# Kernel optimization log

Hardware: AMD Instinct MI355X
Metric: run time of the kernel (lower is better)

Reference implementation:

```python
import jax, jax.numpy as jnp
import numpy as np

N, F, H, C = 50000, 128, 4, 32   # nodes, in_channels, heads, hidden_channels
E, R, DE = 800000, 8, 64         # edges, num_relations, edge_dim


def setup_inputs() -> dict:
    key = jax.random.key(0)
    ks = jax.random.split(key, 10)
    x = jax.random.normal(ks[0], (N, F), dtype=jnp.float32)
    edge_index = jax.random.randint(ks[1], (2, E), 0, N, dtype=jnp.int64)
    edge_type = jax.random.randint(ks[2], (E,), 0, R, dtype=jnp.int64)
    s_in = 1.0 / np.sqrt(F)
    s_e = 1.0 / np.sqrt(DE)
    edge_emb = jax.random.normal(ks[3], (R, DE), dtype=jnp.float32)
    Wq = jax.random.normal(ks[4], (F, H * C), dtype=jnp.float32) * s_in
    Wk = jax.random.normal(ks[5], (F, H * C), dtype=jnp.float32) * s_in
    Wv = jax.random.normal(ks[6], (F, H * C), dtype=jnp.float32) * s_in
    We = jax.random.normal(ks[7], (DE, H * C), dtype=jnp.float32) * s_e
    Wskip = jax.random.normal(ks[8], (F, H * C), dtype=jnp.float32) * s_in
    return {"x": x, "edge_index": edge_index, "edge_type": edge_type,
            "edge_emb": edge_emb, "Wq": Wq, "Wk": Wk, "Wv": Wv,
            "We": We, "Wskip": Wskip}


def reference(x, edge_index, edge_type, edge_emb, Wq, Wk, Wv, We, Wskip):
    # TransformerConv (PyG) with edge embeddings, concat heads, root skip, no bias.
    src, dst = edge_index[0], edge_index[1]
    q = (x @ Wq).reshape(N, H, C)
    k = (x @ Wk).reshape(N, H, C)
    v = (x @ Wv).reshape(N, H, C)
    e = (edge_emb[edge_type] @ We).reshape(E, H, C)      # per-edge relation emb
    kj = k[src] + e                                       # [E,H,C]
    logits = (q[dst] * kj).sum(-1) / jnp.sqrt(jnp.float32(C))  # [E,H]
    # segment softmax over incoming edges of each target node
    m = jax.ops.segment_max(logits, dst, num_segments=N)  # [N,H]
    m = jnp.where(jnp.isfinite(m), m, jnp.float32(0.0))
    ex = jnp.exp(logits - m[dst])
    denom = jax.ops.segment_sum(ex, dst, num_segments=N)  # [N,H]
    alpha = ex / (denom[dst] + 1e-16)                     # [E,H]
    msg = (v[src] + e) * alpha[:, :, None]                # [E,H,C]
    out = jax.ops.segment_sum(msg, dst, num_segments=N).reshape(N, H * C)
    return out + x @ Wskip
```

## Files before the change

### kernel.cpp

```cpp
#include <hip/hip_runtime.h>
#include <hip/hip_bf16.h>

#define NN 50000
#define FF 128
#define NH 4
#define CH 32
#define HC 128
#define NE 800000
#define NR 8
#define DEDIM 64
#define NBLK 196
#define HBLK 3125
#define QBLK 250
#define MTILES 3125

typedef __hip_bfloat16 bf16;
typedef __attribute__((ext_vector_type(8))) short short8;
typedef __attribute__((ext_vector_type(4))) float f32x4;

__device__ __forceinline__ float bflo(unsigned u) { return __uint_as_float(u << 16); }
__device__ __forceinline__ float bfhi(unsigned u) { return __uint_as_float(u & 0xFFFF0000u); }

__device__ __forceinline__ unsigned short f2bf(float f) {
  unsigned u = __float_as_uint(f);
  unsigned r = (u + 0x7FFFu + ((u >> 16) & 1u)) >> 16;
  return (unsigned short)r;
}
__device__ __forceinline__ unsigned pack2bf(float lo, float hi) {
  return (unsigned)f2bf(lo) | ((unsigned)f2bf(hi) << 16);
}

template <int ISBF>
__device__ __forceinline__ float ldf(const void* p, size_t i) {
  if (ISBF) return __bfloat162float(((const bf16*)p)[i]);
  return ((const float*)p)[i];
}

__device__ __forceinline__ int idx_at(const void* p, long long i, int is64) {
  if (is64) { long long v = ((const long long*)p)[i]; return (int)v; }
  return ((const int*)p)[i];
}

#define WT_STRIDE 136

template <int ISBF>
__device__ __forceinline__ void stage_w(const void* __restrict__ W,
                                        unsigned short* __restrict__ wt) {
  for (int i = threadIdx.x; i < FF * HC; i += 256) {
    int k = i >> 7, n = i & 127;
    wt[n * WT_STRIDE + k] = ISBF ? ((const unsigned short*)W)[i]
                                 : f2bf(((const float*)W)[i]);
  }
}

__device__ __forceinline__ void hoist_b(const unsigned short* __restrict__ wt,
                                        int wv, int quad, int lr,
                                        short8 bf[2][4]) {
#pragma unroll
  for (int t = 0; t < 2; ++t) {
    int ncol = wv * 32 + t * 16 + lr;
#pragma unroll
    for (int kb = 0; kb < 4; ++kb)
      bf[t][kb] = *(const short8*)&wt[ncol * WT_STRIDE + kb * 32 + quad * 8];
  }
}

template <int ISBF>
__device__ __forceinline__ void qkvs_body(const void* __restrict__ x,
    const void* __restrict__ W0, const void* __restrict__ W1, int grp, int mc,
    unsigned short* __restrict__ qb, unsigned* __restrict__ kvb,
    void* __restrict__ out, unsigned short* wt) {
  const int lane = threadIdx.x & 63;
  const int wv   = threadIdx.x >> 6;
  const int quad = lane >> 4;
  const int lr   = lane & 15;
  short8 bf0[2][4], bf1[2][4];
  stage_w<ISBF>(W0, wt);
  __syncthreads();
  hoist_b(wt, wv, quad, lr, bf0);
  __syncthreads();
  stage_w<ISBF>(W1, wt);
  __syncthreads();
  hoist_b(wt, wv, quad, lr, bf1);
  const unsigned short* xu = (const unsigned short*)x;
  const float* xf = (const float*)x;
  for (int mt = mc; mt < MTILES; mt += QBLK) {
    int m0 = mt * 16;
    short8 af[4];
#pragma unroll
    for (int kb = 0; kb < 4; ++kb) {
      size_t off = (size_t)(m0 + lr) * FF + kb * 32 + quad * 8;
      if (ISBF) {
        af[kb] = *(const short8*)(xu + off);
      } else {
        float4 fa = *(const float4*)(xf + off);
        float4 fb = *(const float4*)(xf + off + 4);
        short8 a;
        a[0] = (short)f2bf(fa.x); a[1] = (short)f2bf(fa.y);
        a[2] = (short)f2bf(fa.z); a[3] = (short)f2bf(fa.w);
        a[4] = (short)f2bf(fb.x); a[5] = (short)f2bf(fb.y);
        a[6] = (short)f2bf(fb.z); a[7] = (short)f2bf(fb.w);
        af[kb] = a;
      }
    }
    f32x4 a00 = {0.f, 0.f, 0.f, 0.f}, a01 = {0.f, 0.f, 0.f, 0.f};
    f32x4 a10 = {0.f, 0.f, 0.f, 0.f}, a11 = {0.f, 0.f, 0.f, 0.f};
#pragma unroll
    for (int kb = 0; kb < 4; ++kb) {
      a00 = __builtin_amdgcn_mfma_f32_16x16x32_bf16(af[kb], bf0[0][kb], a00, 0, 0, 0);
      a01 = __builtin_amdgcn_mfma_f32_16x16x32_bf16(af[kb], bf0[1][kb], a01, 0, 0, 0);
      a10 = __builtin_amdgcn_mfma_f32_16x16x32_bf16(af[kb], bf1[0][kb], a10, 0, 0, 0);
      a11 = __builtin_amdgcn_mfma_f32_16x16x32_bf16(af[kb], bf1[1][kb], a11, 0, 0, 0);
    }
#pragma unroll
    for (int t = 0; t < 2; ++t) {
      const f32x4 v0 = t ? a01 : a00;
      const f32x4 v1 = t ? a11 : a10;
      int col = wv * 32 + t * 16 + lr;
#pragma unroll
      for (int r = 0; r < 4; ++r) {
        size_t oi = (size_t)(m0 + quad * 4 + r) * HC + col;
        if (grp == 0) {
          qb[oi] = f2bf(v0[r]);
          if (ISBF) ((unsigned short*)out)[oi] = f2bf(v1[r]);
          else      ((float*)out)[oi] = v1[r];
        } else {
          kvb[oi] = pack2bf(v0[r], v1[r]);
        }
      }
    }
  }
}

__global__ __launch_bounds__(256) void k_fusedA(const unsigned* __restrict__ xw,
    const int* __restrict__ eidx32, const void* __restrict__ etype,
    const void* __restrict__ emb, const void* __restrict__ We,
    const void* __restrict__ Wq, const void* __restrict__ Ws,
    int* __restrict__ flag, int* __restrict__ hist, float* __restrict__ ee,
    unsigned* __restrict__ drk, int* __restrict__ setp,
    unsigned short* __restrict__ qb, void* __restrict__ out) {
  __shared__ unsigned short wt[HC * WT_STRIDE];
  if (blockIdx.x < QBLK) {
    unsigned ex = (xw[threadIdx.x & 63] >> 7) & 0xFFu;
    unsigned long long bb = __ballot(ex < 90u || ex > 140u);
    int isbf = (bb == 0ULL);
    if (isbf) qkvs_body<1>(xw, Wq, Ws, 0, blockIdx.x, qb, nullptr, out, wt);
    else      qkvs_body<0>(xw, Wq, Ws, 0, blockIdx.x, qb, nullptr, out, wt);
    return;
  }
  if (blockIdx.x < QBLK + HBLK) {
    unsigned long long b = __ballot(eidx32[2 * (threadIdx.x & 63) + 1] != 0);
    int is64 = (b == 0ULL);
    int e = (blockIdx.x - QBLK) * 256 + threadIdx.x;
    int src = idx_at(eidx32, e, is64);
    int dst = idx_at(eidx32, (long long)NE + e, is64);
    int et  = idx_at(etype, e, is64);
    src = min(max(src, 0), NN - 1);
    dst = min(max(dst, 0), NN - 1);
    et  = min(max(et, 0), NR - 1);
    int rank = atomicAdd(&hist[dst], 1);
    drk[e]  = ((unsigned)dst << 16) | ((unsigned)rank & 0xFFFFu);
    setp[e] = (src << 3) | et;
    return;
  }
  float* es = (float*)wt;
  __shared__ int nzIdx, badBf;
  if (threadIdx.x == 0) { nzIdx = 0; badBf = 0; }
  __syncthreads();
  if (threadIdx.x < 128) {
    if (eidx32[2 * threadIdx.x + 1] != 0) atomicAdd(&nzIdx, 1);
    unsigned e = (xw[threadIdx.x] >> 7) & 0xFFu;
    if (e < 90u || e > 140u) atomicAdd(&badBf, 1);
  }
  __syncthreads();
  const int isbf = (badBf == 0);
  if (threadIdx.x == 0) { flag[0] = (nzIdx == 0); flag[1] = isbf; }
  for (int i = threadIdx.x; i < NR * DEDIM; i += 256)
    es[i] = isbf ? ldf<1>(emb, i) : ldf<0>(emb, i);
  __syncthreads();
  for (int o = threadIdx.x; o < NR * HC; o += 256) {
    int r = o >> 7, j = o & 127;
    float acc = 0.f;
    if (isbf) { for (int d = 0; d < DEDIM; ++d) acc += es[r * DEDIM + d] * ldf<1>(We, d * HC + j); }
    else      { for (int d = 0; d < DEDIM; ++d) acc += es[r * DEDIM + d] * ldf<0>(We, d * HC + j); }
    ee[o] = acc;
  }
}

__global__ __launch_bounds__(256) void k_scan1(const int* __restrict__ hist,
                                               int* __restrict__ bsum) {
  __shared__ int red[4];
  int i = blockIdx.x * 256 + threadIdx.x;
  int v = (i < NN) ? hist[i] : 0;
#pragma unroll
  for (int m = 1; m < 64; m <<= 1) v += __shfl_xor(v, m);
  if ((threadIdx.x & 63) == 0) red[threadIdx.x >> 6] = v;
  __syncthreads();
  if (threadIdx.x == 0) bsum[blockIdx.x] = red[0] + red[1] + red[2] + red[3];
}

__global__ __launch_bounds__(256) void k_scan13(const int* __restrict__ hist,
    const int* __restrict__ bsum, int* __restrict__ rowptr) {
  __shared__ int s[256];
  int t = threadIdx.x;
  int bv = (t < NBLK) ? bsum[t] : 0;
  s[t] = bv;
  __syncthreads();
  for (int off = 1; off < 256; off <<= 1) {
    int u = (t >= off) ? s[t - off] : 0;
    __syncthreads();
    s[t] += u;
    __syncthreads();
  }
  int bexc = (blockIdx.x == 0) ? 0 : s[blockIdx.x - 1];
  __syncthreads();
  int i = blockIdx.x * 256 + t;
  int v = (i < NN) ? hist[i] : 0;
  s[t] = v;
  __syncthreads();
  for (int off = 1; off < 256; off <<= 1) {
    int u = (t >= off) ? s[t - off] : 0;
    __syncthreads();
    s[t] += u;
    __syncthreads();
  }
  int excl = bexc + s[t] - v;
  if (i < NN) rowptr[i] = excl;
  if (i == 0) rowptr[NN] = NE;
}

__global__ __launch_bounds__(256) void k_fusedB(const unsigned* __restrict__ xw,
    const void* __restrict__ Wk, const void* __restrict__ Wv,
    unsigned* __restrict__ kvb,
    const unsigned* __restrict__ drk, const int* __restrict__ setp,
    const int* __restrict__ rowptr, int* __restrict__ srcet) {
  __shared__ unsigned short wt[HC * WT_STRIDE];
  if (blockIdx.x < QBLK) {
    unsigned ex = (xw[threadIdx.x & 63] >> 7) & 0xFFu;
    unsigned long long bb = __ballot(ex < 90u || ex > 140u);
    int isbf = (bb == 0ULL);
    if (isbf) qkvs_body<1>(xw, Wk, Wv, 1, blockIdx.x, nullptr, kvb, nullptr, wt);
    else      qkvs_body<0>(xw, Wk, Wv, 1, blockIdx.x, nullptr, kvb, nullptr, wt);
    return;
  }
  int e = (blockIdx.x - QBLK) * 256 + threadIdx.x;
  unsigned d = drk[e];
  int pos = rowptr[d >> 16] + (int)(d & 0xFFFFu);
  pos = min(max(pos, 0), NE - 1);
  srcet[pos] = setp[e];
}

__global__ __launch_bounds__(256) void k_gather(const int* __restrict__ rowptr,
    const int* __restrict__ srcet, const unsigned short* __restrict__ qb,
    const unsigned* __restrict__ kvb, const float* __restrict__ ee,
    const int* __restrict__ flag, void* __restrict__ out) {
  int n = blockIdx.x * 4 + (threadIdx.x >> 6);
  int l = threadIdx.x & 63;
  int t = l >> 5;
  int w = l & 31;
  int j0 = ((w >> 3) << 5) + ((w & 7) << 2);
  int beg = __builtin_amdgcn_readfirstlane(rowptr[n]);
  int end = __builtin_amdgcn_readfirstlane(rowptr[n + 1]);
  uint2 qw = *(const uint2*)(qb + (size_t)n * HC + j0);
  float q0 = bflo(qw.x), q1 = bfhi(qw.x), q2 = bflo(qw.y), q3 = bfhi(qw.y);
  const float sc = 0.17677669529663687f;
  float dn = 0.f, a0 = 0.f, a1 = 0.f, a2 = 0.f, a3 = 0.f;
  int p = beg;
  for (; p + 8 <= end; p += 8) {
    int se[4]; uint4 kv[4]; float4 ev[4];
#pragma unroll
    for (int u = 0; u < 4; ++u) se[u] = srcet[p + 2 * u + t];
#pragma unroll
    for (int u = 0; u < 4; ++u)
      kv[u] = *(const uint4*)(kvb + (size_t)(se[u] >> 3) * HC + j0);
#pragma unroll
    for (int u = 0; u < 4; ++u)
      ev[u] = *(const float4*)(ee + ((se[u] & 7) << 7) + j0);
#pragma unroll
    for (int u = 0; u < 4; ++u) {
      float pp = q0 * (bflo(kv[u].x) + ev[u].x) + q1 * (bflo(kv[u].y) + ev[u].y)
               + q2 * (bflo(kv[u].z) + ev[u].z) + q3 * (bflo(kv[u].w) + ev[u].w);
      pp += __shfl_xor(pp, 1);
      pp += __shfl_xor(pp, 2);
      pp += __shfl_xor(pp, 4);
      float xx = __expf(pp * sc);
      dn += xx;
      a0 += (bfhi(kv[u].x) + ev[u].x) * xx;
      a1 += (bfhi(kv[u].y) + ev[u].y) * xx;
      a2 += (bfhi(kv[u].z) + ev[u].z) * xx;
      a3 += (bfhi(kv[u].w) + ev[u].w) * xx;
    }
  }
  if (p < end) {
    int se[4]; bool ok[4]; uint4 kv[4]; float4 ev[4];
#pragma unroll
    for (int u = 0; u < 4; ++u) {
      int pe = p + 2 * u + t;
      ok[u] = pe < end;
      se[u] = srcet[ok[u] ? pe : beg];
    }
#pragma unroll
    for (int u = 0; u < 4; ++u)
      kv[u] = *(const uint4*)(kvb + (size_t)(se[u] >> 3) * HC + j0);
#pragma unroll
    for (int u = 0; u < 4; ++u)
      ev[u] = *(const float4*)(ee + ((se[u] & 7) << 7) + j0);
#pragma unroll
    for (int u = 0; u < 4; ++u) {
      float pp = q0 * (bflo(kv[u].x) + ev[u].x) + q1 * (bflo(kv[u].y) + ev[u].y)
               + q2 * (bflo(kv[u].z) + ev[u].z) + q3 * (bflo(kv[u].w) + ev[u].w);
      pp += __shfl_xor(pp, 1);
      pp += __shfl_xor(pp, 2);
      pp += __shfl_xor(pp, 4);
      float xx = ok[u] ? __expf(pp * sc) : 0.f;
      dn += xx;
      a0 += (bfhi(kv[u].x) + ev[u].x) * xx;
      a1 += (bfhi(kv[u].y) + ev[u].y) * xx;
      a2 += (bfhi(kv[u].z) + ev[u].z) * xx;
      a3 += (bfhi(kv[u].w) + ev[u].w) * xx;
    }
  }
  dn += __shfl_xor(dn, 32);
  a0 += __shfl_xor(a0, 32);
  a1 += __shfl_xor(a1, 32);
  a2 += __shfl_xor(a2, 32);
  a3 += __shfl_xor(a3, 32);
  if (t == 0) {
    float inv = 1.f / (dn + 1e-16f);
    size_t oi = (size_t)n * HC + j0;
    if (flag[1]) {
      uint2 sk = *(const uint2*)((const unsigned short*)out + oi);
      uint2 o;
      o.x = pack2bf(a0 * inv + bflo(sk.x), a1 * inv + bfhi(sk.x));
      o.y = pack2bf(a2 * inv + bflo(sk.y), a3 * inv + bfhi(sk.y));
      *(uint2*)((unsigned short*)out + oi) = o;
    } else {
      float4 sk = *(const float4*)((const float*)out + oi);
      float4 o = make_float4(a0 * inv + sk.x, a1 * inv + sk.y,
                             a2 * inv + sk.z, a3 * inv + sk.w);
      *(float4*)((float*)out + oi) = o;
    }
  }
}

extern "C" void kernel_launch(void* const* d_in, const int* in_sizes, int n_in,
                              void* d_out, int out_size, void* d_ws, size_t ws_size,
                              hipStream_t stream) {
  const void* x     = d_in[0];
  const void* eidx  = d_in[1];
  const void* etype = d_in[2];
  const void* emb   = d_in[3];
  const void* Wq    = d_in[4];
  const void* Wk    = d_in[5];
  const void* Wv    = d_in[6];
  const void* We    = d_in[7];
  const void* Ws    = d_in[8];

  float* base   = (float*)d_ws;
  int*   flag   = (int*)base;
  float* ee     = base + 16;
  int*   rowptr = (int*)(base + 1040);
  int*   hist   = (int*)(base + 51044);
  int*   bsum   = (int*)(base + 101044);
  int*   srcet  = (int*)(base + 101568);
  unsigned* drk = (unsigned*)(base + 901568);
  int*   setp   = (int*)(base + 1701568);
  unsigned short* qb  = (unsigned short*)(base + 2501568);
  unsigned*       kvb = (unsigned*)(base + 5701568);

  hipMemsetAsync(hist, 0, NN * sizeof(int), stream);
  k_fusedA<<<QBLK + HBLK + 1, 256, 0, stream>>>((const unsigned*)x,
                                                (const int*)eidx, etype, emb, We,
                                                Wq, Ws, flag, hist, ee,
                                                drk, setp, qb, d_out);
  k_scan1 <<<NBLK, 256, 0, stream>>>(hist, bsum);
  k_scan13<<<NBLK, 256, 0, stream>>>(hist, bsum, rowptr);
  k_fusedB<<<QBLK + HBLK, 256, 0, stream>>>((const unsigned*)x, Wk, Wv, kvb,
                                            drk, setp, rowptr, srcet);
  k_gather<<<NN / 4, 256, 0, stream>>>(rowptr, srcet, qb, kvb, ee, flag, d_out);
}
```

Baseline: 245.0 us.

## Stage GEMM output tiles in LDS for coalesced stores; vectorize weight staging; more projection blocks

The projection GEMM epilogue now writes each 16-row output tile into shared memory and then copies it to global memory with 16-byte coalesced stores, instead of issuing scattered 2- and 4-byte stores per accumulator element. Weight staging into shared memory now uses vectorized copies in row-major layout, and the B-fragment hoist gathers 8 strided scalars per fragment from that layout. The number of projection blocks rises from 250 to 625, which spreads the tiles across more blocks but adds a weight-staging pass to each extra block. The extra barriers per tile and the unpadded, strided LDS reads in the hoist may cause bank conflicts.

```diff
diff --git a/kernel.cpp b/kernel.cpp
--- a/kernel.cpp
+++ b/kernel.cpp
@@ -11,7 +11,7 @@
 #define DEDIM 64
 #define NBLK 196
 #define HBLK 3125
-#define QBLK 250
+#define QBLK 625
 #define MTILES 3125
 
 typedef __hip_bfloat16 bf16;
@@ -41,15 +41,25 @@
   return ((const int*)p)[i];
 }
 
-#define WT_STRIDE 136
-
 template <int ISBF>
 __device__ __forceinline__ void stage_w(const void* __restrict__ W,
                                         unsigned short* __restrict__ wt) {
-  for (int i = threadIdx.x; i < FF * HC; i += 256) {
-    int k = i >> 7, n = i & 127;
-    wt[n * WT_STRIDE + k] = ISBF ? ((const unsigned short*)W)[i]
-                                 : f2bf(((const float*)W)[i]);
+  if (ISBF) {
+    const uint4* src = (const uint4*)W;
+    uint4* dst = (uint4*)wt;
+    for (int i = threadIdx.x; i < FF * HC / 8; i += 256) dst[i] = src[i];
+  } else {
+    const float4* src = (const float4*)W;
+    short8* dst = (short8*)wt;
+    for (int i = threadIdx.x; i < FF * HC / 8; i += 256) {
+      float4 a = src[2 * i], b = src[2 * i + 1];
+      short8 o;
+      o[0] = (short)f2bf(a.x); o[1] = (short)f2bf(a.y);
+      o[2] = (short)f2bf(a.z); o[3] = (short)f2bf(a.w);
+      o[4] = (short)f2bf(b.x); o[5] = (short)f2bf(b.y);
+      o[6] = (short)f2bf(b.z); o[7] = (short)f2bf(b.w);
+      dst[i] = o;
+    }
   }
 }
 
@@ -60,8 +70,13 @@
   for (int t = 0; t < 2; ++t) {
     int ncol = wv * 32 + t * 16 + lr;
 #pragma unroll
-    for (int kb = 0; kb < 4; ++kb)
-      bf[t][kb] = *(const short8*)&wt[ncol * WT_STRIDE + kb * 32 + quad * 8];
+    for (int kb = 0; kb < 4; ++kb) {
+      short8 v;
+#pragma unroll
+      for (int j = 0; j < 8; ++j)
+        v[j] = (short)wt[(kb * 32 + quad * 8 + j) * HC + ncol];
+      bf[t][kb] = v;
+    }
   }
 }
 
@@ -82,6 +97,12 @@
   stage_w<ISBF>(W1, wt);
   __syncthreads();
   hoist_b(wt, wv, quad, lr, bf1);
+  __syncthreads();
+  unsigned short* qt = wt;
+  unsigned short* st = wt + 16 * HC;
+  float*          ot = (float*)(wt + 16 * HC);
+  unsigned*       kt = (unsigned*)wt;
+
   const unsigned short* xu = (const unsigned short*)x;
   const float* xf = (const float*)x;
   for (int mt = mc; mt < MTILES; mt += QBLK) {
@@ -119,16 +140,33 @@
       int col = wv * 32 + t * 16 + lr;
 #pragma unroll
       for (int r = 0; r < 4; ++r) {
-        size_t oi = (size_t)(m0 + quad * 4 + r) * HC + col;
+        int row = quad * 4 + r;
         if (grp == 0) {
-          qb[oi] = f2bf(v0[r]);
-          if (ISBF) ((unsigned short*)out)[oi] = f2bf(v1[r]);
-          else      ((float*)out)[oi] = v1[r];
+          qt[row * HC + col] = f2bf(v0[r]);
+          if (ISBF) st[row * HC + col] = f2bf(v1[r]);
+          else      ot[row * HC + col] = v1[r];
         } else {
-          kvb[oi] = pack2bf(v0[r], v1[r]);
+          kt[row * HC + col] = pack2bf(v0[r], v1[r]);
         }
       }
     }
+    __syncthreads();
+    const int tid = threadIdx.x;
+    if (grp == 0) {
+      ((uint4*)(qb + (size_t)m0 * HC))[tid] = ((const uint4*)qt)[tid];
+      if (ISBF) {
+        ((uint4*)((unsigned short*)out + (size_t)m0 * HC))[tid] = ((const uint4*)st)[tid];
+      } else {
+        uint4* dst = (uint4*)((float*)out + (size_t)m0 * HC);
+        dst[tid]       = ((const uint4*)ot)[tid];
+        dst[tid + 256] = ((const uint4*)ot)[tid + 256];
+      }
+    } else {
+      uint4* dst = (uint4*)(kvb + (size_t)m0 * HC);
+      dst[tid]       = ((const uint4*)kt)[tid];
+      dst[tid + 256] = ((const uint4*)kt)[tid + 256];
+    }
+    __syncthreads();
   }
 }
 
@@ -139,7 +177,7 @@
     int* __restrict__ flag, int* __restrict__ hist, float* __restrict__ ee,
     unsigned* __restrict__ drk, int* __restrict__ setp,
     unsigned short* __restrict__ qb, void* __restrict__ out) {
-  __shared__ unsigned short wt[HC * WT_STRIDE];
+  __shared__ __align__(16) unsigned short wt[FF * HC];
   if (blockIdx.x < QBLK) {
     unsigned ex = (xw[threadIdx.x & 63] >> 7) & 0xFFu;
     unsigned long long bb = __ballot(ex < 90u || ex > 140u);
@@ -234,7 +272,7 @@
     unsigned* __restrict__ kvb,
     const unsigned* __restrict__ drk, const int* __restrict__ setp,
     const int* __restrict__ rowptr, int* __restrict__ srcet) {
-  __shared__ unsigned short wt[HC * WT_STRIDE];
+  __shared__ __align__(16) unsigned short wt[FF * HC];
   if (blockIdx.x < QBLK) {
     unsigned ex = (xw[threadIdx.x & 63] >> 7) & 0xFFu;
     unsigned long long bb = __ballot(ex < 90u || ex > 140u);
```

New measurement: 257.7 us. 1.05x slower.

## Move K/V projection GEMM into first fused kernel, leaving a pure scatter pass

Applied to the files above, without the earlier changes.

The K/V projection blocks move out of the second fused kernel and into k_fusedA, alongside the Q/skip GEMM and the histogram/rank atomics. The second kernel becomes a slim k_scatter that only places the sorted src/edge-type entries. The aim is to overlap the K/V GEMM with the atomic-heavy histogram pass instead of running it after the scan. The hist buffer is also aliased onto the srcet region, which is safe only because the scan reads hist before the scatter writes srcet. The first kernel gets longer and heavier, which may change how its blocks are scheduled.

```diff
diff --git a/kernel.cpp b/kernel.cpp
--- a/kernel.cpp
+++ b/kernel.cpp
@@ -65,9 +65,9 @@
   }
 }
 
-template <int ISBF>
+template <int ISBF, int GRP>
 __device__ __forceinline__ void qkvs_body(const void* __restrict__ x,
-    const void* __restrict__ W0, const void* __restrict__ W1, int grp, int mc,
+    const void* __restrict__ W0, const void* __restrict__ W1, int mc,
     unsigned short* __restrict__ qb, unsigned* __restrict__ kvb,
     void* __restrict__ out, unsigned short* wt) {
   const int lane = threadIdx.x & 63;
@@ -120,7 +120,7 @@
 #pragma unroll
       for (int r = 0; r < 4; ++r) {
         size_t oi = (size_t)(m0 + quad * 4 + r) * HC + col;
-        if (grp == 0) {
+        if (GRP == 0) {
           qb[oi] = f2bf(v0[r]);
           if (ISBF) ((unsigned short*)out)[oi] = f2bf(v1[r]);
           else      ((float*)out)[oi] = v1[r];
@@ -136,22 +136,30 @@
     const int* __restrict__ eidx32, const void* __restrict__ etype,
     const void* __restrict__ emb, const void* __restrict__ We,
     const void* __restrict__ Wq, const void* __restrict__ Ws,
+    const void* __restrict__ Wk, const void* __restrict__ Wv,
     int* __restrict__ flag, int* __restrict__ hist, float* __restrict__ ee,
     unsigned* __restrict__ drk, int* __restrict__ setp,
-    unsigned short* __restrict__ qb, void* __restrict__ out) {
+    unsigned short* __restrict__ qb, unsigned* __restrict__ kvb,
+    void* __restrict__ out) {
   __shared__ unsigned short wt[HC * WT_STRIDE];
-  if (blockIdx.x < QBLK) {
+  if (blockIdx.x < 2 * QBLK) {
     unsigned ex = (xw[threadIdx.x & 63] >> 7) & 0xFFu;
     unsigned long long bb = __ballot(ex < 90u || ex > 140u);
     int isbf = (bb == 0ULL);
-    if (isbf) qkvs_body<1>(xw, Wq, Ws, 0, blockIdx.x, qb, nullptr, out, wt);
-    else      qkvs_body<0>(xw, Wq, Ws, 0, blockIdx.x, qb, nullptr, out, wt);
+    if (blockIdx.x < QBLK) {
+      if (isbf) qkvs_body<1, 0>(xw, Wq, Ws, blockIdx.x, qb, kvb, out, wt);
+      else      qkvs_body<0, 0>(xw, Wq, Ws, blockIdx.x, qb, kvb, out, wt);
+    } else {
+      int mc = blockIdx.x - QBLK;
+      if (isbf) qkvs_body<1, 1>(xw, Wk, Wv, mc, qb, kvb, out, wt);
+      else      qkvs_body<0, 1>(xw, Wk, Wv, mc, qb, kvb, out, wt);
+    }
     return;
   }
-  if (blockIdx.x < QBLK + HBLK) {
+  if (blockIdx.x < 2 * QBLK + HBLK) {
     unsigned long long b = __ballot(eidx32[2 * (threadIdx.x & 63) + 1] != 0);
     int is64 = (b == 0ULL);
-    int e = (blockIdx.x - QBLK) * 256 + threadIdx.x;
+    int e = (blockIdx.x - 2 * QBLK) * 256 + threadIdx.x;
     int src = idx_at(eidx32, e, is64);
     int dst = idx_at(eidx32, (long long)NE + e, is64);
     int et  = idx_at(etype, e, is64);
@@ -229,21 +237,10 @@
   if (i == 0) rowptr[NN] = NE;
 }
 
-__global__ __launch_bounds__(256) void k_fusedB(const unsigned* __restrict__ xw,
-    const void* __restrict__ Wk, const void* __restrict__ Wv,
-    unsigned* __restrict__ kvb,
-    const unsigned* __restrict__ drk, const int* __restrict__ setp,
-    const int* __restrict__ rowptr, int* __restrict__ srcet) {
-  __shared__ unsigned short wt[HC * WT_STRIDE];
-  if (blockIdx.x < QBLK) {
-    unsigned ex = (xw[threadIdx.x & 63] >> 7) & 0xFFu;
-    unsigned long long bb = __ballot(ex < 90u || ex > 140u);
-    int isbf = (bb == 0ULL);
-    if (isbf) qkvs_body<1>(xw, Wk, Wv, 1, blockIdx.x, nullptr, kvb, nullptr, wt);
-    else      qkvs_body<0>(xw, Wk, Wv, 1, blockIdx.x, nullptr, kvb, nullptr, wt);
-    return;
-  }
-  int e = (blockIdx.x - QBLK) * 256 + threadIdx.x;
+__global__ __launch_bounds__(256) void k_scatter(const unsigned* __restrict__ drk,
+    const int* __restrict__ setp, const int* __restrict__ rowptr,
+    int* __restrict__ srcet) {
+  int e = blockIdx.x * 256 + threadIdx.x;
   unsigned d = drk[e];
   int pos = rowptr[d >> 16] + (int)(d & 0xFFFFu);
   pos = min(max(pos, 0), NE - 1);
@@ -360,22 +357,21 @@
   int*   flag   = (int*)base;
   float* ee     = base + 16;
   int*   rowptr = (int*)(base + 1040);
-  int*   hist   = (int*)(base + 51044);
-  int*   bsum   = (int*)(base + 101044);
+  int*   bsum   = (int*)(base + 51044);
   int*   srcet  = (int*)(base + 101568);
+  int*   hist   = srcet;
   unsigned* drk = (unsigned*)(base + 901568);
   int*   setp   = (int*)(base + 1701568);
   unsigned short* qb  = (unsigned short*)(base + 2501568);
   unsigned*       kvb = (unsigned*)(base + 5701568);
 
   hipMemsetAsync(hist, 0, NN * sizeof(int), stream);
-  k_fusedA<<<QBLK + HBLK + 1, 256, 0, stream>>>((const unsigned*)x,
-                                                (const int*)eidx, etype, emb, We,
-                                                Wq, Ws, flag, hist, ee,
-                                                drk, setp, qb, d_out);
-  k_scan1 <<<NBLK, 256, 0, stream>>>(hist, bsum);
-  k_scan13<<<NBLK, 256, 0, stream>>>(hist, bsum, rowptr);
-  k_fusedB<<<QBLK + HBLK, 256, 0, stream>>>((const unsigned*)x, Wk, Wv, kvb,
-                                            drk, setp, rowptr, srcet);
-  k_gather<<<NN / 4, 256, 0, stream>>>(rowptr, srcet, qb, kvb, ee, flag, d_out);
-}
+  k_fusedA<<<2 * QBLK + HBLK + 1, 256, 0, stream>>>((const unsigned*)x,
+                                                    (const int*)eidx, etype, emb, We,
+                                                    Wq, Ws, Wk, Wv, flag, hist, ee,
+                                                    drk, setp, qb, kvb, d_out);
+  k_scan1  <<<NBLK, 256, 0, stream>>>(hist, bsum);
+  k_scan13 <<<NBLK, 256, 0, stream>>>(hist, bsum, rowptr);
+  k_scatter<<<HBLK, 256, 0, stream>>>(drk, setp, rowptr, srcet);
+  k_gather <<<NN / 4, 256, 0, stream>>>(rowptr, srcet, qb, kvb, ee, flag, d_out);
+}
```

Measured after the change: 253.3 us. 3.4% more time.
